# Kernel tuning notes

Hardware: AMD Instinct MI355X
Metric: run time of the kernel (lower is better)

Reference implementation:

```python
import jax, jax.numpy as jnp
import numpy as np

B, N, E, H = 4, 512, 512, 8   # batch, tokens, embedding_channels (=KV_size_S), num_heads
C = 4 * E                      # KV_size_C
D = E // H                     # head dim
EPS = 1e-5                     # InstanceNorm2d default eps


def _inorm(x, axes):
    # InstanceNorm2d (affine=False): normalize over spatial axes with biased variance
    m = jnp.mean(x, axis=axes, keepdims=True)
    v = jnp.var(x, axis=axes, keepdims=True)
    return (x - m) * jax.lax.rsqrt(v + EPS)


def setup_inputs() -> dict:
    key = jax.random.key(0)
    ks = jax.random.split(key, 24)
    s = 0.02
    inp = {
        'emb1': jax.random.normal(ks[0], (B, N, E), jnp.float32),
        'emb2': jax.random.normal(ks[1], (B, N, E), jnp.float32),
        'emb3': jax.random.normal(ks[2], (B, N, E), jnp.float32),
        'emb4': jax.random.normal(ks[3], (B, N, E), jnp.float32),
        'emb_C': jax.random.normal(ks[4], (B, N, C), jnp.float32),
        'Wq1': jax.random.normal(ks[5], (E, E), jnp.float32) * s,
        'Wq2': jax.random.normal(ks[6], (E, E), jnp.float32) * s,
        'Wq3': jax.random.normal(ks[7], (E, E), jnp.float32) * s,
        'Wq4': jax.random.normal(ks[8], (E, E), jnp.float32) * s,
        'Wk': jax.random.normal(ks[9], (E, E), jnp.float32) * s,
        'Wv': jax.random.normal(ks[10], (E, E), jnp.float32) * s,
        'WqC': jax.random.normal(ks[11], (C, C), jnp.float32) * s,
        'WkC': jax.random.normal(ks[12], (C, C), jnp.float32) * s,
        'WvC': jax.random.normal(ks[13], (C, C), jnp.float32) * s,
        'Wo1': jax.random.normal(ks[14], (E, E), jnp.float32) * s,
        'Wo2': jax.random.normal(ks[15], (E, E), jnp.float32) * s,
        'Wo3': jax.random.normal(ks[16], (E, E), jnp.float32) * s,
        'Wo4': jax.random.normal(ks[17], (E, E), jnp.float32) * s,
    }
    return inp


def _heads(x):
    # [B, N, E] -> [B, H, N, D]
    b, n, _ = x.shape
    return x.reshape(b, n, H, D).transpose(0, 2, 1, 3)


def reference(emb1, emb2, emb3, emb4, emb_C,
              Wq1, Wq2, Wq3, Wq4, Wk, Wv, WqC, WkC, WvC,
              Wo1, Wo2, Wo3, Wo4):
    # ---- channel cross-attention ----
    QC = emb_C @ WqC.T            # [B, N, C]
    KC = emb_C @ WkC.T
    VC = emb_C @ WvC.T
    attn_c = jnp.einsum('bnc,bnd->bcd', QC, KC)        # [B, C, C]
    sim_c = jax.nn.softmax(_inorm(attn_c, (1, 2)), axis=-1)  # psi1 + softmax(dim=3)
    ctx_c = jnp.einsum('bcd,bnd->bcn', sim_c, VC)      # [B, C, N]
    T_hat = ctx_c.transpose(0, 2, 1)                   # [B, N, C]
    # split last dim into 4 chunks of E, concat along tokens -> [B, 4N, E]
    KV_S = jnp.concatenate(jnp.split(T_hat, 4, axis=2), axis=1)

    # ---- spatial multi-head cross-attention, shared K/V ----
    K = _heads(KV_S @ Wk.T)       # [B, H, 4N, D]
    V = _heads(KV_S @ Wv.T)

    outs = []
    for emb, Wq, Wo in ((emb1, Wq1, Wo1), (emb2, Wq2, Wo2),
                        (emb3, Wq3, Wo3), (emb4, Wq4, Wo4)):
        Q = _heads(emb @ Wq.T)                          # [B, H, N, D]
        attn = jnp.einsum('bhnd,bhmd->bhnm', Q, K)      # [B, H, N, 4N]
        sim = jax.nn.softmax(_inorm(attn, (2, 3)), axis=-1)  # psi2 + softmax
        ctx = jnp.einsum('bhnm,bhmd->bhnd', sim, V)     # [B, H, N, D]
        ctx = ctx.transpose(0, 2, 1, 3).reshape(emb.shape[0], emb.shape[1], E)
        outs.append(ctx @ Wo.T)
    return tuple(outs)
```

## Files before the change

kernel.cpp:

```cpp
#include <hip/hip_runtime.h>
#include <hip/hip_bf16.h>
#include <hip/hip_fp16.h>

typedef long long i64;
typedef unsigned int u32;
typedef __attribute__((ext_vector_type(8))) short bf16x8;
typedef __attribute__((ext_vector_type(4))) float f32x4;

#define MFMA_BF16 __builtin_amdgcn_mfma_f32_16x16x32_bf16

__device__ __forceinline__ void glds16(const void* g, void* l){
    __builtin_amdgcn_global_load_lds((const __attribute__((address_space(1))) u32*)g,
                                     (__attribute__((address_space(3))) u32*)l, 16, 0, 0);
}
__device__ __forceinline__ void split1(float x, ushort& h, ushort& l){
    unsigned b = __float_as_uint(x);
    h = (ushort)(b >> 16);
    float hf = __uint_as_float(b & 0xFFFF0000u);
    float lf = x - hf;
    l = (ushort)(__float_as_uint(lf) >> 16);
}
__device__ __forceinline__ float bfpair(ushort h, ushort l){
    return __uint_as_float((u32)h << 16) + __uint_as_float((u32)l << 16);
}
__device__ __forceinline__ void ld4h(const __half* p, float v[4]){
    const __half2* q = (const __half2*)p;
    __half2 a = q[0], b = q[1];
    v[0]=__low2float(a); v[1]=__high2float(a);
    v[2]=__low2float(b); v[3]=__high2float(b);
}
__device__ __forceinline__ bf16x8 fragS(const ushort* P, int row, int g){
    return *(const bf16x8*)&P[row*64 + (((g) ^ (row & 7)) << 3)];
}

struct P4 { const void* p[4]; };
struct I4 { int v[4]; };

struct PSJobs { const float* s[13]; ushort* d[13]; int st[14]; };
__global__ __launch_bounds__(256) void presplit(PSJobs J){
    int bid = blockIdx.x, j = 0;
    while (bid >= J.st[j+1]) ++j;
    i64 base = (i64)(bid - J.st[j])*2048 + threadIdx.x*8;
    i64 loOff = (i64)(J.st[j+1] - J.st[j])*2048;
    const float* sp = J.s[j]; ushort* dp = J.d[j];
    float4 a = *(const float4*)&sp[base];
    float4 b = *(const float4*)&sp[base+4];
    float v[8] = {a.x,a.y,a.z,a.w,b.x,b.y,b.z,b.w};
    ushort h[8], l[8];
    #pragma unroll
    for (int t = 0; t < 8; ++t) split1(v[t], h[t], l[t]);
    *(ushort4*)&dp[base]         = make_ushort4(h[0],h[1],h[2],h[3]);
    *(ushort4*)&dp[base+4]       = make_ushort4(h[4],h[5],h[6],h[7]);
    *(ushort4*)&dp[loOff+base]   = make_ushort4(l[0],l[1],l[2],l[3]);
    *(ushort4*)&dp[loOff+base+4] = make_ushort4(l[4],l[5],l[6],l[7]);
}

template<bool AF16, int OUT>
__global__ __launch_bounds__(256) void gemm_ps(
    P4 Ap, P4 Bp, P4 Cp, I4 cmode, float* __restrict__ stats,
    int K, int zdiv,
    i64 ab2, i64 alda, i64 aLo,
    i64 bb2, i64 bldb, i64 bLo,
    i64 cb2, i64 cld, i64 cLo)
{
    __shared__ ushort Ah[2][4096], Al[2][4096], Bh[2][4096], Bl[2][4096];
    __shared__ float sred[4], qred[4];
    const int z = blockIdx.z, z1 = z / zdiv, z2 = z % zdiv;
    const int m0 = blockIdx.y*128, n0 = blockIdx.x*128;
    const int tid = threadIdx.x, lane = tid & 63, wid = tid >> 6;
    const int wm = wid >> 1, wn = wid & 1, fr = lane & 15, kc = lane >> 4;
    const ushort* Aps = (const ushort*)Ap.p[z1] + (i64)z2*ab2 + (i64)m0*alda;
    const __half* Af  = (const __half*)Ap.p[z1] + (i64)z2*ab2 + (i64)m0*alda;
    const ushort* Bps = (const ushort*)Bp.p[z1] + (i64)z2*bb2 + (i64)n0*bldb;

    const int srow = wid*32 + (lane >> 2);
    const int sg   = lane & 3;

    auto stageB = [&](int k0, int pb){
        #pragma unroll
        for (int q = 0; q < 2; ++q) {
            int r  = srow + q*16;
            int gs = sg ^ ((r >> 1) & 3);
            const ushort* sp = Bps + (i64)r*bldb + k0 + gs*8;
            glds16(sp,       &Bh[pb][(wid*32+q*16)*32]);
            glds16(sp + bLo, &Bl[pb][(wid*32+q*16)*32]);
        }
    };
    auto stageA = [&](int k0, int pb){
        if (!AF16) {
            #pragma unroll
            for (int q = 0; q < 2; ++q) {
                int r  = srow + q*16;
                int gs = sg ^ ((r >> 1) & 3);
                const ushort* sp = Aps + (i64)r*alda + k0 + gs*8;
                glds16(sp,       &Ah[pb][(wid*32+q*16)*32]);
                glds16(sp + aLo, &Al[pb][(wid*32+q*16)*32]);
            }
        } else {
            #pragma unroll
            for (int s4 = 0; s4 < 4; ++s4) {
                int v = tid + s4*256; int r = v >> 3, c4 = v & 7;
                float vals[4]; ld4h(&Af[(i64)r*alda + k0 + c4*4], vals);
                ushort h[4], l[4];
                #pragma unroll
                for (int t = 0; t < 4; ++t) split1(vals[t], h[t], l[t]);
                int pc = ((((c4 >> 1) ^ ((r >> 1) & 3)) << 1) | (c4 & 1)) * 4;
                *(ushort4*)&Ah[pb][r*32 + pc] = make_ushort4(h[0],h[1],h[2],h[3]);
                *(ushort4*)&Al[pb][r*32 + pc] = make_ushort4(l[0],l[1],l[2],l[3]);
            }
        }
    };
    auto rd = [&](const ushort* P, int row, int kcc)->bf16x8 {
        return *(const bf16x8*)&P[row*32 + ((kcc ^ ((row >> 1) & 3)) << 3)];
    };

    f32x4 acc[4][4];
    #pragma unroll
    for (int i = 0; i < 4; ++i)
        #pragma unroll
        for (int j = 0; j < 4; ++j) acc[i][j] = (f32x4){0.f,0.f,0.f,0.f};

    const int NT = K >> 5;
    stageA(0, 0); stageB(0, 0);
    __syncthreads();

    for (int t = 0; t < NT; ++t) {
        const int cur = t & 1;
        if (t + 1 < NT) {
            stageA((t+1) << 5, cur ^ 1);
            stageB((t+1) << 5, cur ^ 1);
        }
        bf16x8 a_h[4], a_l[4], b_h[4], b_l[4];
        #pragma unroll
        for (int i = 0; i < 4; ++i) {
            int row = wm*64 + i*16 + fr;
            a_h[i] = rd(Ah[cur], row, kc);
            a_l[i] = rd(Al[cur], row, kc);
        }
        #pragma unroll
        for (int j = 0; j < 4; ++j) {
            int row = wn*64 + j*16 + fr;
            b_h[j] = rd(Bh[cur], row, kc);
            b_l[j] = rd(Bl[cur], row, kc);
        }
        #pragma unroll
        for (int i = 0; i < 4; ++i)
            #pragma unroll
            for (int j = 0; j < 4; ++j) {
                acc[i][j] = MFMA_BF16(a_h[i], b_h[j], acc[i][j], 0, 0, 0);
                acc[i][j] = MFMA_BF16(a_h[i], b_l[j], acc[i][j], 0, 0, 0);
                acc[i][j] = MFMA_BF16(a_l[i], b_h[j], acc[i][j], 0, 0, 0);
            }
        __syncthreads();
    }

    const i64 cbase = (i64)z2*cb2;
    if (OUT == 0) {
        float* C = (float*)Cp.p[z1];
        #pragma unroll
        for (int i = 0; i < 4; ++i)
            #pragma unroll
            for (int j = 0; j < 4; ++j)
                #pragma unroll
                for (int r = 0; r < 4; ++r) {
                    int m = m0 + wm*64 + i*16 + kc*4 + r;
                    int n = n0 + wn*64 + j*16 + fr;
                    C[cbase + (i64)m*cld + n] = acc[i][j][r];
                }
    } else if (OUT == 1) {
        ushort* C = (ushort*)Cp.p[z1];
        const int cfg = cmode.v[z1];
        const int tr = cfg >> 30;
        const i64 ldv = cfg & 0x3FFFFFFF;
        #pragma unroll
        for (int i = 0; i < 4; ++i)
            #pragma unroll
            for (int j = 0; j < 4; ++j)
                #pragma unroll
                for (int r = 0; r < 4; ++r) {
                    int m = m0 + wm*64 + i*16 + kc*4 + r;
                    int n = n0 + wn*64 + j*16 + fr;
                    ushort h, l; split1(acc[i][j][r], h, l);
                    i64 off = cbase + (tr ? (i64)n*ldv + m : (i64)m*ldv + n);
                    C[off] = h; C[off + cLo] = l;
                }
    } else if (OUT == 2) {
        __half* C = (__half*)Cp.p[z1];
        float ls = 0.f, lq = 0.f;
        #pragma unroll
        for (int i = 0; i < 4; ++i)
            #pragma unroll
            for (int j = 0; j < 4; ++j)
                #pragma unroll
                for (int r = 0; r < 4; ++r) {
                    int m = m0 + wm*64 + i*16 + kc*4 + r;
                    int n = n0 + wn*64 + j*16 + fr;
                    float v = acc[i][j][r];
                    ls += v; lq += v*v;
                    C[cbase + (i64)m*cld + n] = __float2half(v);
                }
        #pragma unroll
        for (int off = 32; off; off >>= 1) { ls += __shfl_xor(ls, off); lq += __shfl_xor(lq, off); }
        if (lane == 0) { sred[wid] = ls; qred[wid] = lq; }
        __syncthreads();
        if (tid == 0) {
            atomicAdd(&stats[2*z],   sred[0]+sred[1]+sred[2]+sred[3]);
            atomicAdd(&stats[2*z+1], qred[0]+qred[1]+qred[2]+qred[3]);
        }
    } else {
        ushort* C = (ushort*)Cp.p[z1];
        #pragma unroll
        for (int i = 0; i < 4; ++i)
            #pragma unroll
            for (int j = 0; j < 4; ++j)
                #pragma unroll
                for (int r = 0; r < 4; ++r) {
                    int m = m0 + wm*64 + i*16 + kc*4 + r;
                    int n = n0 + wn*64 + j*16 + fr;
                    ushort h, l; split1(acc[i][j][r], h, l);
                    i64 off = cbase + ((i64)(m >> 9) << 18) + ((i64)n << 9) + (m & 511);
                    C[off] = h; C[off + cLo] = l;
                }
    }
}

__global__ __launch_bounds__(256) void softmax_rows(
    __half* __restrict__ attn, const float* __restrict__ stats,
    int rows_per_stat, float inv_count)
{
    const int ROWLEN = 2048;
    const int row = blockIdx.x;
    const int sidx = row / rows_per_stat;
    float sm = stats[2*sidx], sq = stats[2*sidx+1];
    float mean = sm * inv_count;
    float var = fmaxf(sq * inv_count - mean*mean, 0.f);
    float scale = rsqrtf(var + 1e-5f);
    __half* rp = attn + (i64)row * ROWLEN;
    const int tid = threadIdx.x;
    float v[8]; float mx = -3.4e38f;
    #pragma unroll
    for (int s = 0; s < 8; ++s) { float x = __half2float(rp[tid + s*256]) * scale; v[s] = x; mx = fmaxf(mx, x); }
    #pragma unroll
    for (int off = 32; off; off >>= 1) mx = fmaxf(mx, __shfl_xor(mx, off));
    __shared__ float red[4];
    if ((tid & 63) == 0) red[tid >> 6] = mx;
    __syncthreads();
    mx = fmaxf(fmaxf(red[0], red[1]), fmaxf(red[2], red[3]));
    float ls = 0.f;
    #pragma unroll
    for (int s = 0; s < 8; ++s) { float e = __expf(v[s] - mx); v[s] = e; ls += e; }
    #pragma unroll
    for (int off = 32; off; off >>= 1) ls += __shfl_xor(ls, off);
    __syncthreads();
    if ((tid & 63) == 0) red[tid >> 6] = ls;
    __syncthreads();
    float inv = 1.f / (red[0] + red[1] + red[2] + red[3]);
    #pragma unroll
    for (int s = 0; s < 8; ++s) rp[tid + s*256] = __float2half(v[s] * inv);
}

__global__ __launch_bounds__(256) void gram64(
    const ushort* __restrict__ hi, i64 loOff, float* __restrict__ parts,
    i64 bstride, i64 zs2)
{
    __shared__ float T[16][68];
    __shared__ float csred[4][64];
    const int z = blockIdx.x;
    const int tid = threadIdx.x;
    const ushort* base = hi + (i64)(z>>3)*bstride + (i64)blockIdx.z*zs2
                       + (i64)blockIdx.y*256*512 + (z&7)*64;
    float g[4][4] = {{0.f}};
    float cs = 0.f;
    const int sr = tid >> 4, sc = (tid & 15) * 4;
    const int col = tid & 63, qq = tid >> 6;
    for (int grp = 0; grp < 16; ++grp) {
        i64 idx = (i64)(grp*16 + sr)*512 + sc;
        ushort4 hv = *(const ushort4*)&base[idx];
        ushort4 lv = *(const ushort4*)&base[loOff + idx];
        float4 ld;
        ld.x = bfpair(hv.x, lv.x); ld.y = bfpair(hv.y, lv.y);
        ld.z = bfpair(hv.z, lv.z); ld.w = bfpair(hv.w, lv.w);
        __syncthreads();
        *(float4*)&T[sr][sc] = ld;
        __syncthreads();
        #pragma unroll
        for (int rr = 0; rr < 16; ++rr) {
            const float4 a = *(const float4*)&T[rr][sr*4];
            const float4 b = *(const float4*)&T[rr][sc];
            g[0][0]+=a.x*b.x; g[0][1]+=a.x*b.y; g[0][2]+=a.x*b.z; g[0][3]+=a.x*b.w;
            g[1][0]+=a.y*b.x; g[1][1]+=a.y*b.y; g[1][2]+=a.y*b.z; g[1][3]+=a.y*b.w;
            g[2][0]+=a.z*b.x; g[2][1]+=a.z*b.y; g[2][2]+=a.z*b.z; g[2][3]+=a.z*b.w;
            g[3][0]+=a.w*b.x; g[3][1]+=a.w*b.y; g[3][2]+=a.w*b.z; g[3][3]+=a.w*b.w;
        }
        cs += T[qq*4+0][col] + T[qq*4+1][col] + T[qq*4+2][col] + T[qq*4+3][col];
    }
    float* outp = parts + (i64)((blockIdx.z*gridDim.y + blockIdx.y)*gridDim.x + blockIdx.x)*4160;
    #pragma unroll
    for (int x = 0; x < 4; ++x)
        #pragma unroll
        for (int y = 0; y < 4; ++y)
            outp[(sr*4+x)*64 + sc + y] = g[x][y];
    csred[qq][col] = cs;
    __syncthreads();
    if (tid < 64) outp[4096 + tid] = csred[0][tid]+csred[1][tid]+csred[2][tid]+csred[3][tid];
}

__global__ __launch_bounds__(256) void fin_stats(
    const float* __restrict__ gq, const float* __restrict__ gk,
    float* __restrict__ ss)
{
    const int z = blockIdx.x, s = blockIdx.y;
    const int tid = threadIdx.x;
    const int lane = tid & 63, wid = tid >> 6;
    const float* q0 = gq + (i64)((s*2+0)*32 + z)*4160;
    const float* q1 = gq + (i64)((s*2+1)*32 + z)*4160;
    float p2 = 0.f;
    for (int i = tid; i < 4096; i += 256) {
        float a = q0[i] + q1[i];
        float b = 0.f;
        #pragma unroll
        for (int c = 0; c < 8; ++c) b += gk[(i64)(c*32 + z)*4160 + i];
        p2 += a*b;
    }
    float p1 = 0.f;
    if (tid < 64) {
        float a = q0[4096+tid] + q1[4096+tid];
        float b = 0.f;
        #pragma unroll
        for (int c = 0; c < 8; ++c) b += gk[(i64)(c*32 + z)*4160 + 4096 + tid];
        p1 = a*b;
    }
    #pragma unroll
    for (int off = 32; off; off >>= 1) { p2 += __shfl_xor(p2, off); p1 += __shfl_xor(p1, off); }
    __shared__ float r2[4], r1[4];
    if (lane == 0) { r2[wid] = p2; r1[wid] = p1; }
    __syncthreads();
    if (tid == 0) {
        float S2 = r2[0]+r2[1]+r2[2]+r2[3];
        float S1 = r1[0]+r1[1]+r1[2]+r1[3];
        const float inv = 1.f/1048576.f;
        float mu = S1*inv;
        float var = fmaxf(S2*inv - mu*mu, 0.f);
        float sc = rsqrtf(var + 1e-5f);
        ss[(s*32+z)*2] = sc;
        ss[(s*32+z)*2+1] = sc*mu;
    }
}

__global__ __launch_bounds__(256) void flash_ps(
    const ushort* __restrict__ Qp, const ushort* __restrict__ Kp,
    const ushort* __restrict__ Vtp, const float* __restrict__ ss,
    ushort* __restrict__ ctxp)
{
    __shared__ ushort QPh[4096], QPl[4096];
    __shared__ ushort Kh[4096], Kl[4096];
    __shared__ ushort Vh[2][4096], Vl[2][4096];
    __shared__ float denl[2][64];
    const int qt = blockIdx.x, zz = blockIdx.y, s = blockIdx.z;
    const int b = zz >> 3, hD = (zz & 7) * 64;
    const float scale = ss[(s*32+zz)*2], shift = ss[(s*32+zz)*2+1];
    const ushort* Qb = Qp + (i64)s*2097152 + (i64)b*262144 + (i64)(qt*64)*512 + hD;
    const ushort* Kb = Kp + (i64)b*1048576 + hD;
    const ushort* Vb = Vtp + (i64)b*1048576 + (i64)hD*2048;
    const int tid = threadIdx.x, lane = tid & 63, wid = tid >> 6;
    const int wq = wid >> 1, wk = wid & 1, fr = lane & 15, kc = lane >> 4;

    auto stage64 = [&](const ushort* src, i64 ld, i64 lo, ushort* Lh, ushort* Ll){
        #pragma unroll
        for (int q = 0; q < 2; ++q) {
            int rb = wid*16 + q*8;
            int r = rb + (lane >> 3);
            int gs = (lane & 7) ^ (r & 7);
            const ushort* p = src + (i64)r*ld + gs*8;
            glds16(p,      &Lh[rb*64]);
            glds16(p + lo, &Ll[rb*64]);
        }
    };

    stage64(Qb, 512, 1048576, QPh, QPl);
    stage64(Kb, 512, 4194304, Kh, Kl);
    stage64(Vb, 2048, 4194304, Vh[0], Vl[0]);
    __syncthreads();

    bf16x8 qh[2][2], ql[2][2];
    #pragma unroll
    for (int i = 0; i < 2; ++i)
        #pragma unroll
        for (int ks = 0; ks < 2; ++ks) {
            int row = wq*32 + i*16 + fr;
            qh[i][ks] = fragS(QPh, row, ks*4 + kc);
            ql[i][ks] = fragS(QPl, row, ks*4 + kc);
        }
    __syncthreads();

    f32x4 ctx[2][2];
    #pragma unroll
    for (int i = 0; i < 2; ++i)
        #pragma unroll
        for (int j = 0; j < 2; ++j) ctx[i][j] = (f32x4){0.f,0.f,0.f,0.f};
    float den_lr[2][4] = {{0.f}};

    for (int t = 0; t < 32; ++t) {
        f32x4 sacc[2][2];
        #pragma unroll
        for (int i = 0; i < 2; ++i)
            #pragma unroll
            for (int j = 0; j < 2; ++j) sacc[i][j] = (f32x4){0.f,0.f,0.f,0.f};
        #pragma unroll
        for (int ks = 0; ks < 2; ++ks) {
            bf16x8 khf[2], klf[2];
            #pragma unroll
            for (int j = 0; j < 2; ++j) {
                int row = wk*32 + j*16 + fr;
                khf[j] = fragS(Kh, row, ks*4 + kc);
                klf[j] = fragS(Kl, row, ks*4 + kc);
            }
            #pragma unroll
            for (int i = 0; i < 2; ++i)
                #pragma unroll
                for (int j = 0; j < 2; ++j) {
                    sacc[i][j] = MFMA_BF16(qh[i][ks], khf[j], sacc[i][j], 0, 0, 0);
                    sacc[i][j] = MFMA_BF16(qh[i][ks], klf[j], sacc[i][j], 0, 0, 0);
                    sacc[i][j] = MFMA_BF16(ql[i][ks], khf[j], sacc[i][j], 0, 0, 0);
                }
        }
        #pragma unroll
        for (int i = 0; i < 2; ++i)
            #pragma unroll
            for (int j = 0; j < 2; ++j)
                #pragma unroll
                for (int r = 0; r < 4; ++r) {
                    float p = __expf(sacc[i][j][r]*scale - shift);
                    den_lr[i][r] += p;
                    ushort h, l; split1(p, h, l);
                    int row = wq*32 + i*16 + kc*4 + r;
                    int col = wk*32 + j*16 + fr;
                    int pos = row*64 + ((((col>>3) ^ (row&7)) << 3) | (col & 7));
                    QPh[pos] = h; QPl[pos] = l;
                }
        __syncthreads();
        if (t + 1 < 32) {
            stage64(Kb + (i64)((t+1)*64)*512, 512, 4194304, Kh, Kl);
            stage64(Vb + (t+1)*64, 2048, 4194304, Vh[(t+1)&1], Vl[(t+1)&1]);
        }
        #pragma unroll
        for (int ks = 0; ks < 2; ++ks) {
            bf16x8 vhf[2], vlf[2], pah[2], pal[2];
            #pragma unroll
            for (int j = 0; j < 2; ++j) {
                int row = wk*32 + j*16 + fr;
                vhf[j] = fragS(Vh[t&1], row, ks*4 + kc);
                vlf[j] = fragS(Vl[t&1], row, ks*4 + kc);
            }
            #pragma unroll
            for (int i = 0; i < 2; ++i) {
                int row = wq*32 + i*16 + fr;
                pah[i] = fragS(QPh, row, ks*4 + kc);
                pal[i] = fragS(QPl, row, ks*4 + kc);
            }
            #pragma unroll
            for (int i = 0; i < 2; ++i)
                #pragma unroll
                for (int j = 0; j < 2; ++j) {
                    ctx[i][j] = MFMA_BF16(pah[i], vhf[j], ctx[i][j], 0, 0, 0);
                    ctx[i][j] = MFMA_BF16(pah[i], vlf[j], ctx[i][j], 0, 0, 0);
                    ctx[i][j] = MFMA_BF16(pal[i], vhf[j], ctx[i][j], 0, 0, 0);
                }
        }
        __syncthreads();
    }

    #pragma unroll
    for (int i = 0; i < 2; ++i)
        #pragma unroll
        for (int r = 0; r < 4; ++r) {
            float d = den_lr[i][r];
            d += __shfl_xor(d, 1); d += __shfl_xor(d, 2);
            d += __shfl_xor(d, 4); d += __shfl_xor(d, 8);
            if (fr == 0) denl[wk][wq*32 + i*16 + kc*4 + r] = d;
        }
    __syncthreads();
    ushort* Cb = ctxp + (i64)s*2097152 + (i64)b*262144;
    #pragma unroll
    for (int i = 0; i < 2; ++i)
        #pragma unroll
        for (int j = 0; j < 2; ++j)
            #pragma unroll
            for (int r = 0; r < 4; ++r) {
                int row = wq*32 + i*16 + kc*4 + r;
                int col = wk*32 + j*16 + fr;
                float dv = denl[0][row] + denl[1][row];
                ushort h, l; split1(ctx[i][j][r] / dv, h, l);
                i64 off = (i64)(qt*64 + row)*512 + hD + col;
                Cb[off] = h; Cb[off + 1048576] = l;
            }
}

static inline P4 p4x(const void* a, const void* b, const void* c, const void* d){
    P4 x; x.p[0]=a; x.p[1]=b; x.p[2]=c; x.p[3]=d; return x;
}
static inline P4 p4x(const void* a){ return p4x(a,a,a,a); }
static inline I4 i4x(int a, int b, int c, int d){ I4 x; x.v[0]=a; x.v[1]=b; x.v[2]=c; x.v[3]=d; return x; }
#define TRC(ld) ((1<<30)|(ld))

extern "C" void kernel_launch(void* const* d_in, const int* in_sizes, int n_in,
                              void* d_out, int out_size, void* d_ws, size_t ws_size,
                              hipStream_t stream)
{
    (void)in_sizes; (void)n_in; (void)out_size;
    const float* emb[4] = {(const float*)d_in[0], (const float*)d_in[1],
                           (const float*)d_in[2], (const float*)d_in[3]};
    const float* embC = (const float*)d_in[4];
    const float* Wq[4] = {(const float*)d_in[5], (const float*)d_in[6],
                          (const float*)d_in[7], (const float*)d_in[8]};
    const float* Wk  = (const float*)d_in[9];
    const float* Wv  = (const float*)d_in[10];
    const float* WqC = (const float*)d_in[11];
    const float* WkC = (const float*)d_in[12];
    const float* WvC = (const float*)d_in[13];
    const float* Wo[4] = {(const float*)d_in[14], (const float*)d_in[15],
                          (const float*)d_in[16], (const float*)d_in[17]};
    float* out = (float*)d_out;

    char* ws = (char*)d_ws;
    const size_t MB = 1024*1024;
    if (ws_size < 128*MB + 512) return;
    auto U = [&](size_t mb){ return (ushort*)(ws + mb*MB); };
    float* stats = (float*)(ws + 122*MB);
    float* ssbuf = (float*)(ws + 122*MB + 1024);
    float* GKp   = (float*)(ws + 48*MB);
    float* GQp   = (float*)(ws + 53*MB);
    __half* scores = (__half*)(ws + 16*MB);

    hipMemsetAsync(stats, 0, 512, stream);

    {
        PSJobs J;
        const float* srcs[13] = {embC, WqC, WkC, WvC, Wk, Wv,
                                 Wq[0],Wq[1],Wq[2],Wq[3], Wo[0],Wo[1],Wo[2]};
        ushort* dsts[13] = {U(0),U(16),U(32),U(48),U(64),U(65),
                            U(66),U(67),U(68),U(69), U(70),U(71),U(72)};
        int blks[13] = {2048,2048,2048,2048,128,128, 128,128,128,128, 128,128,128};
        int a = 0;
        for (int j = 0; j < 13; ++j) { J.s[j]=srcs[j]; J.d[j]=dsts[j]; J.st[j]=a; a+=blks[j]; }
        J.st[13] = a;
        presplit<<<dim3(a), 256, 0, stream>>>(J);
    }
    gemm_ps<false,1><<<dim3(16, 4, 12), 256, 0, stream>>>(
        p4x(U(0)), p4x(U(16), U(32), U(48), U(48)), p4x(U(74), U(90), U(106), U(106)),
        i4x(TRC(512), TRC(512), 2048, 2048), nullptr, 2048, 4,
        1048576, 2048, 4194304,   0, 2048, 4194304,   1048576, 0, 4194304);
    {
        PSJobs J;
        const float* srcs[13] = {emb[0], emb[1], emb[2], emb[3], Wo[3],
                                 nullptr,nullptr,nullptr,nullptr,nullptr,nullptr,nullptr,nullptr};
        ushort* dsts[13] = {U(0), U(4), U(8), U(12), U(73),
                            nullptr,nullptr,nullptr,nullptr,nullptr,nullptr,nullptr,nullptr};
        int blks[5] = {512,512,512,512,128};
        int a = 0;
        for (int j = 0; j < 5; ++j) { J.s[j]=srcs[j]; J.d[j]=dsts[j]; J.st[j]=a; a+=blks[j]; }
        for (int j = 5; j < 14; ++j) J.st[j] = a;
        presplit<<<dim3(a), 256, 0, stream>>>(J);
    }
    gemm_ps<false,2><<<dim3(16, 16, 4), 256, 0, stream>>>(
        p4x(U(74)), p4x(U(90)), p4x(scores), i4x(0,0,0,0), stats, 512, 4,
        1048576, 512, 4194304,   1048576, 512, 4194304,   4194304, 2048, 0);
    softmax_rows<<<dim3(4*2048), 256, 0, stream>>>(scores, stats, 2048, 1.f/4194304.f);
    gemm_ps<true,3><<<dim3(4, 16, 4), 256, 0, stream>>>(
        p4x(scores), p4x(U(106)), p4x(U(48)), i4x(0,0,0,0), nullptr, 2048, 4,
        4194304, 2048, 0,   1048576, 2048, 4194304,   1048576, 0, 4194304);
    gemm_ps<false,1><<<dim3(4, 16, 8), 256, 0, stream>>>(
        p4x(U(48)), p4x(U(64), U(65), U(65), U(65)), p4x(U(74), U(90), U(90), U(90)),
        i4x(512, TRC(2048), 0, 0), nullptr, 512, 4,
        1048576, 512, 4194304,   0, 512, 262144,   1048576, 0, 4194304);
    gemm_ps<false,1><<<dim3(4, 4, 16), 256, 0, stream>>>(
        p4x(U(0), U(4), U(8), U(12)), p4x(U(66), U(67), U(68), U(69)),
        p4x(U(106), U(110), U(114), U(118)),
        i4x(512,512,512,512), nullptr, 512, 4,
        262144, 512, 1048576,   0, 512, 262144,   262144, 0, 1048576);
    gram64<<<dim3(32, 8, 1), 256, 0, stream>>>(U(74), 4194304, GKp, 1048576, 0);
    gram64<<<dim3(32, 2, 4), 256, 0, stream>>>(U(106), 1048576, GQp, 262144, 2097152);
    fin_stats<<<dim3(32, 4), 256, 0, stream>>>(GQp, GKp, ssbuf);
    flash_ps<<<dim3(8, 32, 4), 256, 0, stream>>>(U(106), U(74), U(90), ssbuf, U(16));
    gemm_ps<false,0><<<dim3(4, 4, 16), 256, 0, stream>>>(
        p4x(U(16), U(20), U(24), U(28)), p4x(U(70), U(71), U(72), U(73)),
        p4x(out, out + 1048576, out + 2097152, out + 3145728),
        i4x(0,0,0,0), nullptr, 512, 4,
        262144, 512, 1048576,   0, 512, 262144,   262144, 512, 1048576);
}
```

Before: 708.5 us.

## Deepen GEMM and flash pipelines with explicit waitcnt barriers; presplit softmax output

The GEMM main loop now prefetches two k-tiles ahead using async global-to-LDS loads and waits on them with explicit vmcnt and raw barriers instead of full __syncthreads. MFMA blocks are wrapped in setprio. The flash kernel double-buffers K as well as V and issues each next-next tile load right after the barrier that frees its buffer. Softmax now writes bf16 hi/lo split planes directly, so the context GEMM no longer converts fp16 to split bf16 inside its inner loop. This drops the per-iteration half-to-bf16 split and its VALU cost, in exchange for extra memory traffic for the low plane and reliance on hand-counted vmcnt values being correct.

```diff
diff --git a/kernel.cpp b/kernel.cpp
--- a/kernel.cpp
+++ b/kernel.cpp
@@ -8,6 +8,10 @@
 typedef __attribute__((ext_vector_type(4))) float f32x4;
 
 #define MFMA_BF16 __builtin_amdgcn_mfma_f32_16x16x32_bf16
+#define VMCNT(n)  asm volatile("s_waitcnt vmcnt(" #n ")" ::: "memory")
+#define LGKM0     asm volatile("s_waitcnt lgkmcnt(0)" ::: "memory")
+#define SBAR      __builtin_amdgcn_s_barrier()
+#define SCHED0    __builtin_amdgcn_sched_barrier(0)
 
 __device__ __forceinline__ void glds16(const void* g, void* l){
     __builtin_amdgcn_global_load_lds((const __attribute__((address_space(1))) u32*)g,
@@ -22,12 +26,6 @@
 }
 __device__ __forceinline__ float bfpair(ushort h, ushort l){
     return __uint_as_float((u32)h << 16) + __uint_as_float((u32)l << 16);
-}
-__device__ __forceinline__ void ld4h(const __half* p, float v[4]){
-    const __half2* q = (const __half2*)p;
-    __half2 a = q[0], b = q[1];
-    v[0]=__low2float(a); v[1]=__high2float(a);
-    v[2]=__low2float(b); v[3]=__high2float(b);
 }
 __device__ __forceinline__ bf16x8 fragS(const ushort* P, int row, int g){
     return *(const bf16x8*)&P[row*64 + (((g) ^ (row & 7)) << 3)];
@@ -55,7 +53,7 @@
     *(ushort4*)&dp[loOff+base+4] = make_ushort4(l[4],l[5],l[6],l[7]);
 }
 
-template<bool AF16, int OUT>
+template<int OUT>
 __global__ __launch_bounds__(256) void gemm_ps(
     P4 Ap, P4 Bp, P4 Cp, I4 cmode, float* __restrict__ stats,
     int K, int zdiv,
@@ -70,44 +68,22 @@
     const int tid = threadIdx.x, lane = tid & 63, wid = tid >> 6;
     const int wm = wid >> 1, wn = wid & 1, fr = lane & 15, kc = lane >> 4;
     const ushort* Aps = (const ushort*)Ap.p[z1] + (i64)z2*ab2 + (i64)m0*alda;
-    const __half* Af  = (const __half*)Ap.p[z1] + (i64)z2*ab2 + (i64)m0*alda;
     const ushort* Bps = (const ushort*)Bp.p[z1] + (i64)z2*bb2 + (i64)n0*bldb;
 
     const int srow = wid*32 + (lane >> 2);
     const int sg   = lane & 3;
 
-    auto stageB = [&](int k0, int pb){
+    auto stageAB = [&](int k0, int pb){
         #pragma unroll
         for (int q = 0; q < 2; ++q) {
             int r  = srow + q*16;
             int gs = sg ^ ((r >> 1) & 3);
-            const ushort* sp = Bps + (i64)r*bldb + k0 + gs*8;
-            glds16(sp,       &Bh[pb][(wid*32+q*16)*32]);
-            glds16(sp + bLo, &Bl[pb][(wid*32+q*16)*32]);
-        }
-    };
-    auto stageA = [&](int k0, int pb){
-        if (!AF16) {
-            #pragma unroll
-            for (int q = 0; q < 2; ++q) {
-                int r  = srow + q*16;
-                int gs = sg ^ ((r >> 1) & 3);
-                const ushort* sp = Aps + (i64)r*alda + k0 + gs*8;
-                glds16(sp,       &Ah[pb][(wid*32+q*16)*32]);
-                glds16(sp + aLo, &Al[pb][(wid*32+q*16)*32]);
-            }
-        } else {
-            #pragma unroll
-            for (int s4 = 0; s4 < 4; ++s4) {
-                int v = tid + s4*256; int r = v >> 3, c4 = v & 7;
-                float vals[4]; ld4h(&Af[(i64)r*alda + k0 + c4*4], vals);
-                ushort h[4], l[4];
-                #pragma unroll
-                for (int t = 0; t < 4; ++t) split1(vals[t], h[t], l[t]);
-                int pc = ((((c4 >> 1) ^ ((r >> 1) & 3)) << 1) | (c4 & 1)) * 4;
-                *(ushort4*)&Ah[pb][r*32 + pc] = make_ushort4(h[0],h[1],h[2],h[3]);
-                *(ushort4*)&Al[pb][r*32 + pc] = make_ushort4(l[0],l[1],l[2],l[3]);
-            }
+            const ushort* sa = Aps + (i64)r*alda + k0 + gs*8;
+            glds16(sa,       &Ah[pb][(wid*32+q*16)*32]);
+            glds16(sa + aLo, &Al[pb][(wid*32+q*16)*32]);
+            const ushort* sb = Bps + (i64)r*bldb + k0 + gs*8;
+            glds16(sb,       &Bh[pb][(wid*32+q*16)*32]);
+            glds16(sb + bLo, &Bl[pb][(wid*32+q*16)*32]);
         }
     };
     auto rd = [&](const ushort* P, int row, int kcc)->bf16x8 {
@@ -121,15 +97,12 @@
         for (int j = 0; j < 4; ++j) acc[i][j] = (f32x4){0.f,0.f,0.f,0.f};
 
     const int NT = K >> 5;
-    stageA(0, 0); stageB(0, 0);
-    __syncthreads();
+    stageAB(0, 0); stageAB(32, 1);
 
     for (int t = 0; t < NT; ++t) {
         const int cur = t & 1;
-        if (t + 1 < NT) {
-            stageA((t+1) << 5, cur ^ 1);
-            stageB((t+1) << 5, cur ^ 1);
-        }
+        if (t + 1 < NT) { VMCNT(8); } else { VMCNT(0); }
+        SBAR;
         bf16x8 a_h[4], a_l[4], b_h[4], b_l[4];
         #pragma unroll
         for (int i = 0; i < 4; ++i) {
@@ -143,6 +116,7 @@
             b_h[j] = rd(Bh[cur], row, kc);
             b_l[j] = rd(Bl[cur], row, kc);
         }
+        __builtin_amdgcn_s_setprio(1);
         #pragma unroll
         for (int i = 0; i < 4; ++i)
             #pragma unroll
@@ -151,7 +125,11 @@
                 acc[i][j] = MFMA_BF16(a_h[i], b_l[j], acc[i][j], 0, 0, 0);
                 acc[i][j] = MFMA_BF16(a_l[i], b_h[j], acc[i][j], 0, 0, 0);
             }
-        __syncthreads();
+        __builtin_amdgcn_s_setprio(0);
+        LGKM0;
+        SBAR;
+        SCHED0;
+        if (t + 2 < NT) stageAB((t+2) << 5, cur);
     }
 
     const i64 cbase = (i64)z2*cb2;
@@ -225,8 +203,8 @@
 }
 
 __global__ __launch_bounds__(256) void softmax_rows(
-    __half* __restrict__ attn, const float* __restrict__ stats,
-    int rows_per_stat, float inv_count)
+    __half* __restrict__ attn, ushort* __restrict__ lo,
+    const float* __restrict__ stats, int rows_per_stat, float inv_count)
 {
     const int ROWLEN = 2048;
     const int row = blockIdx.x;
@@ -236,6 +214,8 @@
     float var = fmaxf(sq * inv_count - mean*mean, 0.f);
     float scale = rsqrtf(var + 1e-5f);
     __half* rp = attn + (i64)row * ROWLEN;
+    ushort* hp = (ushort*)rp;
+    ushort* lp = lo + (i64)row * ROWLEN;
     const int tid = threadIdx.x;
     float v[8]; float mx = -3.4e38f;
     #pragma unroll
@@ -256,7 +236,10 @@
     __syncthreads();
     float inv = 1.f / (red[0] + red[1] + red[2] + red[3]);
     #pragma unroll
-    for (int s = 0; s < 8; ++s) rp[tid + s*256] = __float2half(v[s] * inv);
+    for (int s = 0; s < 8; ++s) {
+        ushort h, l; split1(v[s] * inv, h, l);
+        hp[tid + s*256] = h; lp[tid + s*256] = l;
+    }
 }
 
 __global__ __launch_bounds__(256) void gram64(
@@ -353,9 +336,8 @@
     ushort* __restrict__ ctxp)
 {
     __shared__ ushort QPh[4096], QPl[4096];
-    __shared__ ushort Kh[4096], Kl[4096];
+    __shared__ ushort Kh[2][4096], Kl[2][4096];
     __shared__ ushort Vh[2][4096], Vl[2][4096];
-    __shared__ float denl[2][64];
     const int qt = blockIdx.x, zz = blockIdx.y, s = blockIdx.z;
     const int b = zz >> 3, hD = (zz & 7) * 64;
     const float scale = ss[(s*32+zz)*2], shift = ss[(s*32+zz)*2+1];
@@ -378,10 +360,9 @@
     };
 
     stage64(Qb, 512, 1048576, QPh, QPl);
-    stage64(Kb, 512, 4194304, Kh, Kl);
+    stage64(Kb, 512, 4194304, Kh[0], Kl[0]);
     stage64(Vb, 2048, 4194304, Vh[0], Vl[0]);
-    __syncthreads();
-
+    VMCNT(8); SBAR;
     bf16x8 qh[2][2], ql[2][2];
     #pragma unroll
     for (int i = 0; i < 2; ++i)
@@ -391,7 +372,10 @@
             qh[i][ks] = fragS(QPh, row, ks*4 + kc);
             ql[i][ks] = fragS(QPl, row, ks*4 + kc);
         }
-    __syncthreads();
+    LGKM0; SBAR;
+    SCHED0;
+    stage64(Kb + (i64)64*512, 512, 4194304, Kh[1], Kl[1]);
+    stage64(Vb + 64, 2048, 4194304, Vh[1], Vl[1]);
 
     f32x4 ctx[2][2];
     #pragma unroll
@@ -401,6 +385,9 @@
     float den_lr[2][4] = {{0.f}};
 
     for (int t = 0; t < 32; ++t) {
+        const int cur = t & 1;
+        if (t < 31) { VMCNT(8); } else { VMCNT(0); }
+        SBAR;
         f32x4 sacc[2][2];
         #pragma unroll
         for (int i = 0; i < 2; ++i)
@@ -412,9 +399,10 @@
             #pragma unroll
             for (int j = 0; j < 2; ++j) {
                 int row = wk*32 + j*16 + fr;
-                khf[j] = fragS(Kh, row, ks*4 + kc);
-                klf[j] = fragS(Kl, row, ks*4 + kc);
+                khf[j] = fragS(Kh[cur], row, ks*4 + kc);
+                klf[j] = fragS(Kl[cur], row, ks*4 + kc);
             }
+            __builtin_amdgcn_s_setprio(1);
             #pragma unroll
             for (int i = 0; i < 2; ++i)
                 #pragma unroll
@@ -423,6 +411,7 @@
                     sacc[i][j] = MFMA_BF16(qh[i][ks], klf[j], sacc[i][j], 0, 0, 0);
                     sacc[i][j] = MFMA_BF16(ql[i][ks], khf[j], sacc[i][j], 0, 0, 0);
                 }
+            __builtin_amdgcn_s_setprio(0);
         }
         #pragma unroll
         for (int i = 0; i < 2; ++i)
@@ -438,19 +427,17 @@
                     int pos = row*64 + ((((col>>3) ^ (row&7)) << 3) | (col & 7));
                     QPh[pos] = h; QPl[pos] = l;
                 }
-        __syncthreads();
-        if (t + 1 < 32) {
-            stage64(Kb + (i64)((t+1)*64)*512, 512, 4194304, Kh, Kl);
-            stage64(Vb + (t+1)*64, 2048, 4194304, Vh[(t+1)&1], Vl[(t+1)&1]);
-        }
+        LGKM0; SBAR;
+        SCHED0;
+        if (t < 30) stage64(Kb + (i64)((t+2)*64)*512, 512, 4194304, Kh[cur], Kl[cur]);
         #pragma unroll
         for (int ks = 0; ks < 2; ++ks) {
             bf16x8 vhf[2], vlf[2], pah[2], pal[2];
             #pragma unroll
             for (int j = 0; j < 2; ++j) {
                 int row = wk*32 + j*16 + fr;
-                vhf[j] = fragS(Vh[t&1], row, ks*4 + kc);
-                vlf[j] = fragS(Vl[t&1], row, ks*4 + kc);
+                vhf[j] = fragS(Vh[cur], row, ks*4 + kc);
+                vlf[j] = fragS(Vl[cur], row, ks*4 + kc);
             }
             #pragma unroll
             for (int i = 0; i < 2; ++i) {
@@ -458,6 +445,7 @@
                 pah[i] = fragS(QPh, row, ks*4 + kc);
                 pal[i] = fragS(QPl, row, ks*4 + kc);
             }
+            __builtin_amdgcn_s_setprio(1);
             #pragma unroll
             for (int i = 0; i < 2; ++i)
                 #pragma unroll
@@ -466,10 +454,14 @@
                     ctx[i][j] = MFMA_BF16(pah[i], vlf[j], ctx[i][j], 0, 0, 0);
                     ctx[i][j] = MFMA_BF16(pal[i], vhf[j], ctx[i][j], 0, 0, 0);
                 }
-        }
-        __syncthreads();
-    }
-
+            __builtin_amdgcn_s_setprio(0);
+        }
+        LGKM0; SBAR;
+        SCHED0;
+        if (t < 30) stage64(Vb + (t+2)*64, 2048, 4194304, Vh[cur], Vl[cur]);
+    }
+
+    float* denf = (float*)QPl;
     #pragma unroll
     for (int i = 0; i < 2; ++i)
         #pragma unroll
@@ -477,7 +469,7 @@
             float d = den_lr[i][r];
             d += __shfl_xor(d, 1); d += __shfl_xor(d, 2);
             d += __shfl_xor(d, 4); d += __shfl_xor(d, 8);
-            if (fr == 0) denl[wk][wq*32 + i*16 + kc*4 + r] = d;
+            if (fr == 0) denf[wk*64 + wq*32 + i*16 + kc*4 + r] = d;
         }
     __syncthreads();
     ushort* Cb = ctxp + (i64)s*2097152 + (i64)b*262144;
@@ -489,7 +481,7 @@
             for (int r = 0; r < 4; ++r) {
                 int row = wq*32 + i*16 + kc*4 + r;
                 int col = wk*32 + j*16 + fr;
-                float dv = denl[0][row] + denl[1][row];
+                float dv = denf[row] + denf[64 + row];
                 ushort h, l; split1(ctx[i][j][r] / dv, h, l);
                 i64 off = (i64)(qt*64 + row)*512 + hD + col;
                 Cb[off] = h; Cb[off + 1048576] = l;
@@ -546,7 +538,7 @@
         J.st[13] = a;
         presplit<<<dim3(a), 256, 0, stream>>>(J);
     }
-    gemm_ps<false,1><<<dim3(16, 4, 12), 256, 0, stream>>>(
+    gemm_ps<1><<<dim3(16, 4, 12), 256, 0, stream>>>(
         p4x(U(0)), p4x(U(16), U(32), U(48), U(48)), p4x(U(74), U(90), U(106), U(106)),
         i4x(TRC(512), TRC(512), 2048, 2048), nullptr, 2048, 4,
         1048576, 2048, 4194304,   0, 2048, 4194304,   1048576, 0, 4194304);
@@ -562,18 +554,18 @@
         for (int j = 5; j < 14; ++j) J.st[j] = a;
         presplit<<<dim3(a), 256, 0, stream>>>(J);
     }
-    gemm_ps<false,2><<<dim3(16, 16, 4), 256, 0, stream>>>(
+    gemm_ps<2><<<dim3(16, 16, 4), 256, 0, stream>>>(
         p4x(U(74)), p4x(U(90)), p4x(scores), i4x(0,0,0,0), stats, 512, 4,
         1048576, 512, 4194304,   1048576, 512, 4194304,   4194304, 2048, 0);
-    softmax_rows<<<dim3(4*2048), 256, 0, stream>>>(scores, stats, 2048, 1.f/4194304.f);
-    gemm_ps<true,3><<<dim3(4, 16, 4), 256, 0, stream>>>(
-        p4x(scores), p4x(U(106)), p4x(U(48)), i4x(0,0,0,0), nullptr, 2048, 4,
-        4194304, 2048, 0,   1048576, 2048, 4194304,   1048576, 0, 4194304);
-    gemm_ps<false,1><<<dim3(4, 16, 8), 256, 0, stream>>>(
+    softmax_rows<<<dim3(4*2048), 256, 0, stream>>>(scores, U(74), stats, 2048, 1.f/4194304.f);
+    gemm_ps<3><<<dim3(4, 16, 4), 256, 0, stream>>>(
+        p4x(U(16)), p4x(U(106)), p4x(U(48)), i4x(0,0,0,0), nullptr, 2048, 4,
+        4194304, 2048, 30408704,   1048576, 2048, 4194304,   1048576, 0, 4194304);
+    gemm_ps<1><<<dim3(4, 16, 8), 256, 0, stream>>>(
         p4x(U(48)), p4x(U(64), U(65), U(65), U(65)), p4x(U(74), U(90), U(90), U(90)),
         i4x(512, TRC(2048), 0, 0), nullptr, 512, 4,
         1048576, 512, 4194304,   0, 512, 262144,   1048576, 0, 4194304);
-    gemm_ps<false,1><<<dim3(4, 4, 16), 256, 0, stream>>>(
+    gemm_ps<1><<<dim3(4, 4, 16), 256, 0, stream>>>(
         p4x(U(0), U(4), U(8), U(12)), p4x(U(66), U(67), U(68), U(69)),
         p4x(U(106), U(110), U(114), U(118)),
         i4x(512,512,512,512), nullptr, 512, 4,
@@ -582,7 +574,7 @@
     gram64<<<dim3(32, 2, 4), 256, 0, stream>>>(U(106), 1048576, GQp, 262144, 2097152);
     fin_stats<<<dim3(32, 4), 256, 0, stream>>>(GQp, GKp, ssbuf);
     flash_ps<<<dim3(8, 32, 4), 256, 0, stream>>>(U(106), U(74), U(90), ssbuf, U(16));
-    gemm_ps<false,0><<<dim3(4, 4, 16), 256, 0, stream>>>(
+    gemm_ps<0><<<dim3(4, 4, 16), 256, 0, stream>>>(
         p4x(U(16), U(20), U(24), U(28)), p4x(U(70), U(71), U(72), U(73)),
         p4x(out, out + 1048576, out + 2097152, out + 3145728),
         i4x(0,0,0,0), nullptr, 512, 4,
```

New measurement: 672.7 us. 1.05x faster.
